# Performance work log

Measured on AMD Instinct MI355X. Metric: run time of the kernel, lower is better.

Reference implementation:

```python
import jax, jax.numpy as jnp
import numpy as np

EPS = 1e-6

def rmsnorm(x, w):
    return x * jax.lax.rsqrt(jnp.mean(x * x, axis=-1, keepdims=True) + EPS) * w

def apply_rope(q, k, freqs_cis):
    # q: (B,T,H,D), k: (B,T,Hkv,D), freqs_cis: (T, D//2, 2) = (cos, sin)
    cos = freqs_cis[None, :, None, :, 0]
    sin = freqs_cis[None, :, None, :, 1]
    def rot(t):
        tr = t.reshape(*t.shape[:-1], t.shape[-1] // 2, 2)
        re, im = tr[..., 0], tr[..., 1]
        out = jnp.stack([re * cos - im * sin, re * sin + im * cos], axis=-1)
        return out.reshape(t.shape)
    return rot(q), rot(k)

def swiglu(x, w1, w2, w3):
    # torch Linear: y = x @ W.T ; SwiGLU: (silu(x W1^T) * (x W3^T)) W2^T
    return (jax.nn.silu(x @ w1.T) * (x @ w3.T)) @ w2.T

def setup_inputs() -> dict:
    key = jax.random.key(0)
    ks = jax.random.split(key, 16)
    B, T, C = 4, 2048, 1024
    H, Hkv, D = 16, 4, 64
    E, Hh = 8, 512
    s = 0.02
    # rotary frequencies (theta=10000)
    inv_freq = 1.0 / (10000.0 ** (np.arange(0, D, 2, dtype=np.float32) / D))
    t = np.arange(T, dtype=np.float32)
    ang = np.outer(t, inv_freq)  # (T, D/2)
    freqs_cis = jnp.asarray(np.stack([np.cos(ang), np.sin(ang)], axis=-1))
    return {
        "x": jax.random.normal(ks[0], (B, T, C), jnp.float32),
        "freqs_cis": freqs_cis,
        "norm1_w": jnp.ones((C,), jnp.float32),
        "wq": jax.random.normal(ks[1], (C, C), jnp.float32) * s,
        "wk": jax.random.normal(ks[2], (Hkv * D, C), jnp.float32) * s,
        "wv": jax.random.normal(ks[3], (Hkv * D, C), jnp.float32) * s,
        "wo": jax.random.normal(ks[4], (C, C), jnp.float32) * s,
        "norm2_w": jnp.ones((C,), jnp.float32),
        "gate_w": jax.random.normal(ks[5], (E, C), jnp.float32) * s,
        "sw1": jax.random.normal(ks[6], (Hh, C), jnp.float32) * s,
        "sw2": jax.random.normal(ks[7], (C, Hh), jnp.float32) * s,
        "sw3": jax.random.normal(ks[8], (Hh, C), jnp.float32) * s,
        "ew1": jax.random.normal(ks[9], (E, Hh, C), jnp.float32) * s,
        "ew2": jax.random.normal(ks[10], (E, C, Hh), jnp.float32) * s,
        "ew3": jax.random.normal(ks[11], (E, Hh, C), jnp.float32) * s,
    }

def reference(x, freqs_cis, norm1_w, wq, wk, wv, wo, norm2_w, gate_w,
              sw1, sw2, sw3, ew1, ew2, ew3):
    B, T, C = x.shape
    H, Hkv = 16, 4
    D = C // H
    n_rep = H // Hkv
    E, top_k = gate_w.shape[0], 2

    # --- attention (GQA + RoPE, causal) ---
    xn = rmsnorm(x, norm1_w)
    q = (xn @ wq.T).reshape(B, T, H, D)
    k = (xn @ wk.T).reshape(B, T, Hkv, D)
    v = (xn @ wv.T).reshape(B, T, Hkv, D)
    q, k = apply_rope(q, k, freqs_cis)
    k = jnp.repeat(k, n_rep, axis=2)
    v = jnp.repeat(v, n_rep, axis=2)
    q, k, v = (t.transpose(0, 2, 1, 3) for t in (q, k, v))  # (B,H,T,D)
    scores = jnp.einsum("bhqd,bhkd->bhqk", q, k) / jnp.sqrt(jnp.float32(D))
    causal = jnp.tril(jnp.ones((T, T), bool))
    scores = jnp.where(causal, scores, jnp.finfo(scores.dtype).min)
    attn = jax.nn.softmax(scores, axis=-1)
    y = jnp.einsum("bhqk,bhkd->bhqd", attn, v)
    y = y.transpose(0, 2, 1, 3).reshape(B, T, C) @ wo.T
    x = x + y

    # --- MoE FFN ---
    xn2 = rmsnorm(x, norm2_w)
    shared = swiglu(xn2, sw1, sw2, sw3)
    router_logits = xn2 @ gate_w.T  # (B,T,E)
    top_logits, top_idx = jax.lax.top_k(router_logits, top_k)
    top_w = jax.nn.softmax(top_logits, axis=-1)  # (B,T,top_k)
    # dense per-expert weight, zero where not selected (same math as masked loop)
    w_full = jnp.sum(jax.nn.one_hot(top_idx, E, dtype=xn2.dtype) * top_w[..., None], axis=-2)  # (B,T,E)
    h = jax.nn.silu(jnp.einsum("btc,ehc->bteh", xn2, ew1)) * jnp.einsum("btc,ehc->bteh", xn2, ew3)
    expert_out = jnp.einsum("bteh,ech,bte->btc", h, ew2, w_full)
    x = x + shared + expert_out
    return x, router_logits
```

## Files before the change

### kernel.cpp

```cpp
#include <hip/hip_runtime.h>
#include <math.h>

typedef __bf16 bf16;
typedef bf16 bf16x8 __attribute__((ext_vector_type(8)));
typedef bf16 bf16x4 __attribute__((ext_vector_type(4)));
typedef float f32x4 __attribute__((ext_vector_type(4)));

#define B_    4
#define T_    2048
#define C_    1024
#define H_    16
#define HKV_  4
#define D_    64
#define HH_   512
#define E_    8
#define MTOK  (B_*T_)
#define MAXTILES 144
#define ROWCAP  (MAXTILES*128)

__device__ __forceinline__ f32x4 mfma16(bf16x8 a, bf16x8 b, f32x4 c) {
  return __builtin_amdgcn_mfma_f32_16x16x32_bf16(a, b, c, 0, 0, 0);
}

#define GLOAD16(gsrc, ldst) \
  __builtin_amdgcn_global_load_lds((const __attribute__((address_space(1))) void*)(gsrc), \
                                   (__attribute__((address_space(3))) void*)(ldst), 16, 0, 0)

#define XCD_SWZ(bx, by) \
  const int _nw  = gridDim.x * gridDim.y; \
  const int _bid = blockIdx.y * gridDim.x + blockIdx.x; \
  const int _swz = (_bid & 7) * (_nw >> 3) + (_bid >> 3); \
  const int bx = _swz % gridDim.x; \
  const int by = _swz / gridDim.x;

struct CastSegs {
  const float* src[10];
  bf16* dst[10];
  int prefix[11];
};
__global__ void cast_all_kernel(CastSegs cs) {
  int i = blockIdx.x * 256 + threadIdx.x;
  if (i >= cs.prefix[10]) return;
  int seg = 0;
  #pragma unroll
  for (int k = 0; k < 9; ++k) if (i >= cs.prefix[k+1]) seg = k+1;
  int j = i - cs.prefix[seg];
  float4 v = reinterpret_cast<const float4*>(cs.src[seg])[j];
  bf16x4 o = { (bf16)v.x, (bf16)v.y, (bf16)v.z, (bf16)v.w };
  reinterpret_cast<bf16x4*>(cs.dst[seg])[j] = o;
}

__global__ void rmsnorm_cast_kernel(const float* __restrict__ x, const float* __restrict__ w,
                                    bf16* __restrict__ out) {
  int row = blockIdx.x;
  const float4* xr = reinterpret_cast<const float4*>(x + (size_t)row * C_);
  float4 v = xr[threadIdx.x];
  float ss = v.x*v.x + v.y*v.y + v.z*v.z + v.w*v.w;
  #pragma unroll
  for (int off = 32; off > 0; off >>= 1) ss += __shfl_down(ss, off);
  __shared__ float red[4];
  if ((threadIdx.x & 63) == 0) red[threadIdx.x >> 6] = ss;
  __syncthreads();
  float tot = red[0] + red[1] + red[2] + red[3];
  float scale = rsqrtf(tot * (1.0f / C_) + 1e-6f);
  float4 wv = reinterpret_cast<const float4*>(w)[threadIdx.x];
  bf16x4 o = { (bf16)(v.x*scale*wv.x), (bf16)(v.y*scale*wv.y),
               (bf16)(v.z*scale*wv.z), (bf16)(v.w*scale*wv.w) };
  reinterpret_cast<bf16x4*>(out + (size_t)row * C_)[threadIdx.x] = o;
}

template<int EPI>
__global__ __launch_bounds__(256, 4)
void gemm_bt(const bf16* __restrict__ A, const bf16* __restrict__ W,
             float* __restrict__ D, const float* __restrict__ SRC,
             const float* __restrict__ RS, int rs_stride,
             int M, int N, int K)
{
  XCD_SWZ(bx, by);
  __shared__ __align__(16) bf16 As[128*64];
  __shared__ __align__(16) bf16 Bs[128*64];
  const int tid  = threadIdx.x;
  const int lane = tid & 63;
  const int wid  = tid >> 6;
  const int wr = wid >> 1, wc = wid & 1;
  const int m0 = by * 128;
  const int n0 = bx * 128;
  const int r  = lane & 15;
  const int kg = lane >> 4;
  const int sr8 = lane >> 3;
  const int sc  = ((lane & 7) ^ sr8) * 8;
  const bf16* gA = A + (size_t)(m0 + wid*32 + sr8) * K + sc;
  const bf16* gB = W + (size_t)(n0 + wid*32 + sr8) * K + sc;
  bf16* lA = As + wid * 2048;
  bf16* lB = Bs + wid * 2048;

  f32x4 acc[4][4];
  #pragma unroll
  for (int i = 0; i < 4; ++i)
    #pragma unroll
    for (int j = 0; j < 4; ++j) acc[i][j] = f32x4{0.f,0.f,0.f,0.f};

  for (int kk = 0; kk < K; kk += 64) {
    #pragma unroll
    for (int p = 0; p < 4; ++p) {
      GLOAD16(gA + (size_t)(8*p) * K + kk, lA + p*512);
      GLOAD16(gB + (size_t)(8*p) * K + kk, lB + p*512);
    }
    __syncthreads();
    #pragma unroll
    for (int ks = 0; ks < 2; ++ks) {
      const int sz = (((ks << 2) | kg) ^ (r & 7)) * 8;
      bf16x8 a[4], b[4];
      #pragma unroll
      for (int i = 0; i < 4; ++i)
        a[i] = *reinterpret_cast<const bf16x8*>(&As[(wr*64 + i*16 + r)*64 + sz]);
      #pragma unroll
      for (int j = 0; j < 4; ++j)
        b[j] = *reinterpret_cast<const bf16x8*>(&Bs[(wc*64 + j*16 + r)*64 + sz]);
      #pragma unroll
      for (int i = 0; i < 4; ++i)
        #pragma unroll
        for (int j = 0; j < 4; ++j)
          acc[i][j] = mfma16(a[i], b[j], acc[i][j]);
    }
    __syncthreads();
  }
  const int dr = kg * 4;
  #pragma unroll
  for (int i = 0; i < 4; ++i)
    #pragma unroll
    for (int j = 0; j < 4; ++j)
      #pragma unroll
      for (int rr = 0; rr < 4; ++rr) {
        int m = m0 + wr*64 + i*16 + dr + rr;
        int n = n0 + wc*64 + j*16 + r;
        size_t idx = (size_t)m * N + n;
        float v = acc[i][j][rr];
        if (EPI == 0)      D[idx] = v;
        else if (EPI == 1) D[idx] = SRC[idx] + v;
        else if (EPI == 2) D[idx] += v;
        else               D[idx] += RS[(size_t)m * rs_stride] * v;
      }
}

__global__ __launch_bounds__(256, 4)
void gemm_qkv(const bf16* __restrict__ A, const bf16* __restrict__ W,
              const float* __restrict__ fr,
              bf16* __restrict__ qb, bf16* __restrict__ kb, bf16* __restrict__ vb)
{
  const int K = C_;
  XCD_SWZ(bx, by);
  __shared__ __align__(16) bf16 As[128*64];
  __shared__ __align__(16) bf16 Bs[128*64];
  const int tid  = threadIdx.x;
  const int lane = tid & 63;
  const int wid  = tid >> 6;
  const int wr = wid >> 1, wc = wid & 1;
  const int m0 = by * 128;
  const int n0 = bx * 128;
  const int r  = lane & 15;
  const int kg = lane >> 4;
  const int sr8 = lane >> 3;
  const int sc  = ((lane & 7) ^ sr8) * 8;
  const bf16* gA = A + (size_t)(m0 + wid*32 + sr8) * K + sc;
  const bf16* gB = W + (size_t)(n0 + wid*32 + sr8) * K + sc;
  bf16* lA = As + wid * 2048;
  bf16* lB = Bs + wid * 2048;

  f32x4 acc[4][4];
  #pragma unroll
  for (int i = 0; i < 4; ++i)
    #pragma unroll
    for (int j = 0; j < 4; ++j) acc[i][j] = f32x4{0.f,0.f,0.f,0.f};

  for (int kk = 0; kk < K; kk += 64) {
    #pragma unroll
    for (int p = 0; p < 4; ++p) {
      GLOAD16(gA + (size_t)(8*p) * K + kk, lA + p*512);
      GLOAD16(gB + (size_t)(8*p) * K + kk, lB + p*512);
    }
    __syncthreads();
    #pragma unroll
    for (int ks = 0; ks < 2; ++ks) {
      const int sz = (((ks << 2) | kg) ^ (r & 7)) * 8;
      bf16x8 a[4], b[4];
      #pragma unroll
      for (int i = 0; i < 4; ++i)
        a[i] = *reinterpret_cast<const bf16x8*>(&As[(wr*64 + i*16 + r)*64 + sz]);
      #pragma unroll
      for (int j = 0; j < 4; ++j)
        b[j] = *reinterpret_cast<const bf16x8*>(&Bs[(wc*64 + j*16 + r)*64 + sz]);
      #pragma unroll
      for (int i = 0; i < 4; ++i)
        #pragma unroll
        for (int j = 0; j < 4; ++j)
          acc[i][j] = mfma16(a[i], b[j], acc[i][j]);
    }
    __syncthreads();
  }
  const float QSCALE = 0.125f * 1.44269504088896340736f;
  const int dr = kg * 4;
  #pragma unroll
  for (int i = 0; i < 4; ++i)
    #pragma unroll
    for (int j = 0; j < 4; ++j)
      #pragma unroll
      for (int rr = 0; rr < 4; ++rr) {
        int mrow = m0 + wr*64 + i*16 + dr + rr;
        int b  = mrow >> 11, t = mrow & (T_ - 1);
        int n  = n0 + wc*64 + j*16 + r;
        float v = acc[i][j][rr];
        float p = __shfl_xor(v, 1);
        if (n < 1024) {
          float c = fr[t*64 + (n & 62)], s = fr[t*64 + (n & 62) + 1];
          float ov = (n & 1) ? (p*s + v*c) : (v*c - p*s);
          qb[((size_t)(b*H_ + (n >> 6)) * T_ + t) * 64 + (n & 63)] = (bf16)(ov * QSCALE);
        } else if (n < 1280) {
          float c = fr[t*64 + (n & 62)], s = fr[t*64 + (n & 62) + 1];
          float ov = (n & 1) ? (p*s + v*c) : (v*c - p*s);
          kb[((size_t)(b*HKV_ + ((n - 1024) >> 6)) * T_ + t) * 64 + (n & 63)] = (bf16)ov;
        } else {
          vb[((size_t)(b*HKV_ + ((n - 1280) >> 6)) * T_ + t) * 64 + (n & 63)] = (bf16)v;
        }
      }
}

__global__ __launch_bounds__(256, 4)
void gemm_up_all(const bf16* __restrict__ A,
                 const bf16* __restrict__ SW1, const bf16* __restrict__ SW3,
                 const bf16* __restrict__ EW1, const bf16* __restrict__ EW3,
                 size_t wstride, bf16* __restrict__ sb, bf16* __restrict__ sbm,
                 const int* __restrict__ tb, const int* __restrict__ tki)
{
  const int K = C_;
  XCD_SWZ(bx, by);
  const int y = by;
  const bool dense = (y < 64);
  const bf16 *W1, *W3;
  int rowbase;
  bf16* outp;
  if (dense) {
    W1 = SW1; W3 = SW3; rowbase = y * 128; outp = sb;
  } else {
    int ye = y - 64;
    if (ye >= tb[16]) return;
    int g = 0;
    while (ye >= tb[g + 1]) ++g;
    W1 = EW1 + (size_t)(g & 7) * wstride;
    W3 = EW3 + (size_t)(g & 7) * wstride;
    rowbase = ye * 128; outp = sbm;
  }

  __shared__ __align__(16) bf16 As[128*64];
  __shared__ __align__(16) bf16 W1s[64*64];
  __shared__ __align__(16) bf16 W3s[64*64];
  const int tid  = threadIdx.x;
  const int lane = tid & 63;
  const int wid  = tid >> 6;
  const int wr = wid >> 1, wc = wid & 1;
  const int n0 = bx * 64;
  const int r  = lane & 15;
  const int kg = lane >> 4;
  const int sr8 = lane >> 3;
  const int sc  = ((lane & 7) ^ sr8) * 8;

  int ar[4];
  #pragma unroll
  for (int p = 0; p < 4; ++p) {
    int rw = rowbase + wid*32 + p*8 + sr8;
    ar[p] = dense ? rw : tki[rw];
  }
  const bf16* gW1 = W1 + (size_t)(n0 + wid*16 + sr8) * K + sc;
  const bf16* gW3 = W3 + (size_t)(n0 + wid*16 + sr8) * K + sc;
  bf16* lA  = As  + wid * 2048;
  bf16* lW1 = W1s + wid * 1024;
  bf16* lW3 = W3s + wid * 1024;

  f32x4 acc1[4][2], acc3[4][2];
  #pragma unroll
  for (int i = 0; i < 4; ++i)
    #pragma unroll
    for (int j = 0; j < 2; ++j) { acc1[i][j] = f32x4{0.f,0.f,0.f,0.f}; acc3[i][j] = f32x4{0.f,0.f,0.f,0.f}; }

  for (int kk = 0; kk < K; kk += 64) {
    #pragma unroll
    for (int p = 0; p < 4; ++p)
      GLOAD16(A + (size_t)ar[p] * K + sc + kk, lA + p*512);
    #pragma unroll
    for (int p = 0; p < 2; ++p) {
      GLOAD16(gW1 + (size_t)(8*p) * K + kk, lW1 + p*512);
      GLOAD16(gW3 + (size_t)(8*p) * K + kk, lW3 + p*512);
    }
    __syncthreads();
    #pragma unroll
    for (int ks = 0; ks < 2; ++ks) {
      const int sz = (((ks << 2) | kg) ^ (r & 7)) * 8;
      bf16x8 a[4], w1f[2], w3f[2];
      #pragma unroll
      for (int i = 0; i < 4; ++i)
        a[i] = *reinterpret_cast<const bf16x8*>(&As[(wr*64 + i*16 + r)*64 + sz]);
      #pragma unroll
      for (int j = 0; j < 2; ++j) {
        w1f[j] = *reinterpret_cast<const bf16x8*>(&W1s[(wc*32 + j*16 + r)*64 + sz]);
        w3f[j] = *reinterpret_cast<const bf16x8*>(&W3s[(wc*32 + j*16 + r)*64 + sz]);
      }
      #pragma unroll
      for (int i = 0; i < 4; ++i)
        #pragma unroll
        for (int j = 0; j < 2; ++j) {
          acc1[i][j] = mfma16(a[i], w1f[j], acc1[i][j]);
          acc3[i][j] = mfma16(a[i], w3f[j], acc3[i][j]);
        }
    }
    __syncthreads();
  }
  const int dr = kg * 4;
  #pragma unroll
  for (int i = 0; i < 4; ++i)
    #pragma unroll
    for (int j = 0; j < 2; ++j)
      #pragma unroll
      for (int rr = 0; rr < 4; ++rr) {
        int row = rowbase + wr*64 + i*16 + dr + rr;
        int n = n0 + wc*32 + j*16 + r;
        float v1 = acc1[i][j][rr];
        float v3 = acc3[i][j][rr];
        outp[(size_t)row * HH_ + n] = (bf16)(v1 / (1.f + __expf(-v1)) * v3);
      }
}

__global__ __launch_bounds__(256, 4)
void gemm_down_all(const bf16* __restrict__ Asb, const bf16* __restrict__ Asbm,
                   const bf16* __restrict__ SW2, const bf16* __restrict__ EW2,
                   size_t wstride, bf16* __restrict__ dd, bf16* __restrict__ dwn,
                   const int* __restrict__ tb)
{
  const int K = HH_;
  XCD_SWZ(bx, by);
  const int y = by;
  const bool dense = (y < 64);
  const bf16 *A, *W;
  int rowbase;
  if (dense) {
    A = Asb; W = SW2; rowbase = y * 128;
  } else {
    int ye = y - 64;
    if (ye >= tb[16]) return;
    int g = 0;
    while (ye >= tb[g + 1]) ++g;
    A = Asbm; W = EW2 + (size_t)(g & 7) * wstride;
    rowbase = ye * 128;
  }

  __shared__ __align__(16) bf16 As[128*64];
  __shared__ __align__(16) bf16 Bs[128*64];
  const int tid  = threadIdx.x;
  const int lane = tid & 63;
  const int wid  = tid >> 6;
  const int wr = wid >> 1, wc = wid & 1;
  const int n0 = bx * 128;
  const int r  = lane & 15;
  const int kg = lane >> 4;
  const int sr8 = lane >> 3;
  const int sc  = ((lane & 7) ^ sr8) * 8;
  const bf16* gA = A + (size_t)(rowbase + wid*32 + sr8) * K + sc;
  const bf16* gB = W + (size_t)(n0 + wid*32 + sr8) * K + sc;
  bf16* lA = As + wid * 2048;
  bf16* lB = Bs + wid * 2048;

  f32x4 acc[4][4];
  #pragma unroll
  for (int i = 0; i < 4; ++i)
    #pragma unroll
    for (int j = 0; j < 4; ++j) acc[i][j] = f32x4{0.f,0.f,0.f,0.f};

  for (int kk = 0; kk < K; kk += 64) {
    #pragma unroll
    for (int p = 0; p < 4; ++p) {
      GLOAD16(gA + (size_t)(8*p) * K + kk, lA + p*512);
      GLOAD16(gB + (size_t)(8*p) * K + kk, lB + p*512);
    }
    __syncthreads();
    #pragma unroll
    for (int ks = 0; ks < 2; ++ks) {
      const int sz = (((ks << 2) | kg) ^ (r & 7)) * 8;
      bf16x8 a[4], b[4];
      #pragma unroll
      for (int i = 0; i < 4; ++i)
        a[i] = *reinterpret_cast<const bf16x8*>(&As[(wr*64 + i*16 + r)*64 + sz]);
      #pragma unroll
      for (int j = 0; j < 4; ++j)
        b[j] = *reinterpret_cast<const bf16x8*>(&Bs[(wc*64 + j*16 + r)*64 + sz]);
      #pragma unroll
      for (int i = 0; i < 4; ++i)
        #pragma unroll
        for (int j = 0; j < 4; ++j)
          acc[i][j] = mfma16(a[i], b[j], acc[i][j]);
    }
    __syncthreads();
  }
  const int dr = kg * 4;
  bf16* outp = dense ? dd : dwn;
  #pragma unroll
  for (int i = 0; i < 4; ++i)
    #pragma unroll
    for (int j = 0; j < 4; ++j)
      #pragma unroll
      for (int rr = 0; rr < 4; ++rr) {
        int row = rowbase + wr*64 + i*16 + dr + rr;
        int n = n0 + wc*64 + j*16 + r;
        outp[(size_t)row * C_ + n] = (bf16)acc[i][j][rr];
      }
}

__global__ void moe_scatter_kernel(const bf16* __restrict__ dd,
                                   const bf16* __restrict__ dwn,
                                   const int* __restrict__ t2s,
                                   const float* __restrict__ t2w,
                                   float* __restrict__ out)
{
  int t = blockIdx.x;
  int c = threadIdx.x;
  int s0 = t2s[2*t], s1 = t2s[2*t+1];
  float w0 = t2w[2*t], w1 = t2w[2*t+1];
  bf16x4 dv = reinterpret_cast<const bf16x4*>(dd  + (size_t)t  * C_)[c];
  bf16x4 a  = reinterpret_cast<const bf16x4*>(dwn + (size_t)s0 * C_)[c];
  bf16x4 b  = reinterpret_cast<const bf16x4*>(dwn + (size_t)s1 * C_)[c];
  float4* o = reinterpret_cast<float4*>(out + (size_t)t * C_);
  float4 v = o[c];
  v.x += (float)dv[0] + w0 * (float)a[0] + w1 * (float)b[0];
  v.y += (float)dv[1] + w0 * (float)a[1] + w1 * (float)b[1];
  v.z += (float)dv[2] + w0 * (float)a[2] + w1 * (float)b[2];
  v.w += (float)dv[3] + w0 * (float)a[3] + w1 * (float)b[3];
  o[c] = v;
}

__global__ void transpose_vb_kernel(const bf16* __restrict__ vb, bf16* __restrict__ vt) {
  int idx = blockIdx.x * 256 + threadIdx.x;
  const int total = B_ * HKV_ * 64 * T_;
  if (idx >= total) return;
  int t   = idx & (T_ - 1);
  int d   = (idx >> 11) & 63;
  int kvh = (idx >> 17) & 3;
  int b   = idx >> 19;
  vt[idx] = vb[((size_t)(b*HKV_ + kvh) * T_ + t) * 64 + d];
}

__global__ __launch_bounds__(256, 4)
void flash_attn_kernel(const bf16* __restrict__ Q, const bf16* __restrict__ K,
                       const bf16* __restrict__ VT, bf16* __restrict__ Y)
{
  __shared__ __align__(16) bf16 Klds[64*64];
  __shared__ __align__(16) bf16 Vlds[64*64];
  __shared__ bf16 Plds[4][2][16][72];
  const int tid  = threadIdx.x;
  const int lane = tid & 63;
  const int wid  = tid >> 6;
  const int bid  = blockIdx.x;
  const int gw   = (bid & 7) * 64 + (bid >> 3);
  const int i    = gw & 31;
  const int kvh  = (gw >> 5) & 3;
  const int b    = gw >> 7;
  const int h    = kvh * 4 + wid;
  const int r = lane & 15;
  const int g = lane >> 4;

  const bf16* kptr = K  + ((size_t)(b*HKV_ + kvh) * T_) * 64;
  const bf16* vptr = VT + ((size_t)(b*HKV_ + kvh) * 64) * T_;

  const int srow  = tid >> 3;
  const int schnk = (tid & 7) ^ (srow & 7);
  bf16* kd0 = Klds + wid * 512;
  bf16* kd1 = Klds + 2048 + wid * 512;
  bf16* vd0 = Vlds + wid * 512;
  bf16* vd1 = Vlds + 2048 + wid * 512;

  const int swz0 = ((g    ) ^ (r & 7)) * 8;
  const int swz4 = ((g + 4) ^ (r & 7)) * 8;

  bf16x8 ones;
  #pragma unroll
  for (int z = 0; z < 8; ++z) ones[z] = (bf16)1.0f;

  #pragma unroll
  for (int pi = 0; pi < 2; ++pi) {
    const int qt = pi == 0 ? (63 - i) : i;
    const int qbase = qt * 32;
    const bf16* qptr = Q + ((size_t)(b*H_ + h) * T_ + qbase) * 64;

    bf16x8 aq[2][2];
    #pragma unroll
    for (int u = 0; u < 2; ++u) {
      aq[u][0] = *reinterpret_cast<const bf16x8*>(qptr + (size_t)(u*16 + r) * 64 + g*8);
      aq[u][1] = *reinterpret_cast<const bf16x8*>(qptr + (size_t)(u*16 + r) * 64 + 32 + g*8);
    }

    f32x4 o[2][4], ol[2];
    #pragma unroll
    for (int u = 0; u < 2; ++u) {
      ol[u] = f32x4{0.f,0.f,0.f,0.f};
      #pragma unroll
      for (int q = 0; q < 4; ++q) o[u][q] = f32x4{0.f,0.f,0.f,0.f};
    }

    for (int k0 = 0; k0 < qbase + 32; k0 += 64) {
      GLOAD16(kptr + (size_t)(k0 + srow)      * 64 + schnk*8, kd0);
      GLOAD16(kptr + (size_t)(k0 + 32 + srow) * 64 + schnk*8, kd1);
      GLOAD16(vptr + (size_t)srow        * T_ + k0 + schnk*8, vd0);
      GLOAD16(vptr + (size_t)(32 + srow) * T_ + k0 + schnk*8, vd1);
      __syncthreads();
      f32x4 s[2][4];
      __builtin_amdgcn_s_setprio(1);
      #pragma unroll
      for (int c = 0; c < 4; ++c) {
        const bf16* kb = &Klds[(c*16 + r) * 64];
        bf16x8 kf0 = *reinterpret_cast<const bf16x8*>(kb + swz0);
        bf16x8 kf1 = *reinterpret_cast<const bf16x8*>(kb + swz4);
        #pragma unroll
        for (int u = 0; u < 2; ++u) {
          s[u][c] = f32x4{0.f,0.f,0.f,0.f};
          s[u][c] = mfma16(aq[u][0], kf0, s[u][c]);
          s[u][c] = mfma16(aq[u][1], kf1, s[u][c]);
        }
      }
      __builtin_amdgcn_s_setprio(0);
      #pragma unroll
      for (int u = 0; u < 2; ++u) {
        if (k0 + 63 > qbase + u*16) {
          #pragma unroll
          for (int c = 0; c < 4; ++c)
            #pragma unroll
            for (int rr = 0; rr < 4; ++rr) {
              int q = qbase + u*16 + g*4 + rr;
              int j = k0 + c*16 + r;
              if (j > q) s[u][c][rr] = -__builtin_inff();
            }
        }
      }
      #pragma unroll
      for (int u = 0; u < 2; ++u)
        #pragma unroll
        for (int c = 0; c < 4; ++c)
          #pragma unroll
          for (int rr = 0; rr < 4; ++rr)
            Plds[wid][u][g*4+rr][c*16+r] = (bf16)__builtin_amdgcn_exp2f(s[u][c][rr]);
      bf16x8 pa[2][2];
      #pragma unroll
      for (int u = 0; u < 2; ++u) {
        pa[u][0] = *reinterpret_cast<const bf16x8*>(&Plds[wid][u][r][g*8]);
        pa[u][1] = *reinterpret_cast<const bf16x8*>(&Plds[wid][u][r][32 + g*8]);
      }
      __builtin_amdgcn_s_setprio(1);
      #pragma unroll
      for (int dt = 0; dt < 4; ++dt) {
        const bf16* vb = &Vlds[(dt*16 + r) * 64];
        bf16x8 vf0 = *reinterpret_cast<const bf16x8*>(vb + swz0);
        bf16x8 vf1 = *reinterpret_cast<const bf16x8*>(vb + swz4);
        #pragma unroll
        for (int u = 0; u < 2; ++u) {
          o[u][dt] = mfma16(pa[u][0], vf0, o[u][dt]);
          o[u][dt] = mfma16(pa[u][1], vf1, o[u][dt]);
        }
      }
      #pragma unroll
      for (int u = 0; u < 2; ++u) {
        ol[u] = mfma16(pa[u][0], ones, ol[u]);
        ol[u] = mfma16(pa[u][1], ones, ol[u]);
      }
      __builtin_amdgcn_s_setprio(0);
      __syncthreads();
    }
    #pragma unroll
    for (int u = 0; u < 2; ++u)
      #pragma unroll
      for (int rr = 0; rr < 4; ++rr) {
        float inv = 1.0f / ol[u][rr];
        int t = qbase + u*16 + g*4 + rr;
        bf16* yrow = Y + ((size_t)(b*T_ + t)) * C_ + h*64;
        #pragma unroll
        for (int dt = 0; dt < 4; ++dt)
          yrow[dt*16 + r] = (bf16)(o[u][dt][rr] * inv);
      }
  }
}

__global__ void rms2_router_kernel(const float* __restrict__ x2, const float* __restrict__ nw,
                                   const float* __restrict__ gwf,
                                   bf16* __restrict__ xn_out,
                                   float* __restrict__ logits_out,
                                   int* __restrict__ t2i, float* __restrict__ t2w)
{
  int t = blockIdx.x * 4 + (threadIdx.x >> 6);
  int lane = threadIdx.x & 63;
  const float4* xr = reinterpret_cast<const float4*>(x2 + (size_t)t * C_) + lane * 4;
  float4 v[4];
  float ss = 0.f;
  #pragma unroll
  for (int i = 0; i < 4; ++i) {
    v[i] = xr[i];
    ss += v[i].x*v[i].x + v[i].y*v[i].y + v[i].z*v[i].z + v[i].w*v[i].w;
  }
  #pragma unroll
  for (int off = 32; off > 0; off >>= 1) ss += __shfl_xor(ss, off);
  float scale = rsqrtf(ss * (1.0f / C_) + 1e-6f);
  const float4* nr = reinterpret_cast<const float4*>(nw) + lane * 4;
  float xn[16];
  #pragma unroll
  for (int i = 0; i < 4; ++i) {
    float4 wv = nr[i];
    xn[4*i+0] = v[i].x * scale * wv.x;
    xn[4*i+1] = v[i].y * scale * wv.y;
    xn[4*i+2] = v[i].z * scale * wv.z;
    xn[4*i+3] = v[i].w * scale * wv.w;
  }
  {
    bf16x8 o0, o1;
    #pragma unroll
    for (int i = 0; i < 8; ++i) { o0[i] = (bf16)xn[i]; o1[i] = (bf16)xn[8+i]; }
    bf16x8* dst = reinterpret_cast<bf16x8*>(xn_out + (size_t)t * C_ + lane * 16);
    dst[0] = o0;
    dst[1] = o1;
  }
  float lg[8];
  #pragma unroll
  for (int e = 0; e < 8; ++e) {
    const float4* gr = reinterpret_cast<const float4*>(gwf + (size_t)e * C_) + lane * 4;
    float d = 0.f;
    #pragma unroll
    for (int i = 0; i < 4; ++i) {
      float4 gv = gr[i];
      d += xn[4*i+0]*gv.x + xn[4*i+1]*gv.y + xn[4*i+2]*gv.z + xn[4*i+3]*gv.w;
    }
    #pragma unroll
    for (int off = 1; off < 64; off <<= 1) d += __shfl_xor(d, off);
    lg[e] = d;
  }
  if (lane == 0) {
    #pragma unroll
    for (int e = 0; e < 8; ++e) logits_out[(size_t)t*8 + e] = lg[e];
    int i0 = 0; float b0 = lg[0];
    #pragma unroll
    for (int e = 1; e < 8; ++e) if (lg[e] > b0) { b0 = lg[e]; i0 = e; }
    int i1 = -1; float b1 = -__builtin_inff();
    #pragma unroll
    for (int e = 0; e < 8; ++e) if (e != i0 && lg[e] > b1) { b1 = lg[e]; i1 = e; }
    float w0s = 1.f / (1.f + __expf(b1 - b0));
    float w1s = 1.f - w0s;
    t2i[2*t] = i0;  t2i[2*t+1] = i1;
    t2w[2*t] = w0s; t2w[2*t+1] = w1s;
  }
}

__global__ void moe_build_kernel(const int* __restrict__ t2i, const float* __restrict__ t2w,
                                 int* __restrict__ cnt, int* __restrict__ tb,
                                 int* __restrict__ tki, float* __restrict__ tkw,
                                 int* __restrict__ t2s)
{
  __shared__ int lcnt[16], lbase[17], lcur[16];
  const int tid = threadIdx.x;
  if (tid < 16) { lcnt[tid] = 0; lcur[tid] = 0; }
  __syncthreads();
  for (int t = tid; t < MTOK; t += 1024) {
    atomicAdd(&lcnt[t2i[2*t]],     1);
    atomicAdd(&lcnt[8 + t2i[2*t+1]], 1);
  }
  __syncthreads();
  if (tid == 0) {
    int acc = 0;
    for (int g = 0; g < 16; ++g) { lbase[g] = acc; acc += (lcnt[g] + 127) >> 7; }
    lbase[16] = acc;
    for (int g = 0; g <= 16; ++g) tb[g] = lbase[g];
  }
  if (tid < 16) cnt[tid] = lcnt[tid];
  __syncthreads();
  for (int t = tid; t < MTOK; t += 1024) {
    #pragma unroll
    for (int j = 0; j < 2; ++j) {
      int g = 8*j + t2i[2*t + j];
      int p = atomicAdd(&lcur[g], 1);
      int slot = lbase[g] * 128 + p;
      tki[slot] = t;
      tkw[slot] = t2w[2*t + j];
      t2s[2*t + j] = slot;
    }
  }
  __syncthreads();
  {
    int g = tid >> 6, lane = tid & 63;
    int cs = lcnt[g];
    int ce = (cs + 127) & ~127;
    for (int p = cs + lane; p < ce; p += 64) {
      int slot = lbase[g] * 128 + p;
      tki[slot] = 0;
      tkw[slot] = 0.f;
    }
  }
}

__global__ void silu_mul_kernel(const float* __restrict__ a, const float* __restrict__ bsrc,
                                bf16* __restrict__ out, int n4)
{
  int i = blockIdx.x * 256 + threadIdx.x;
  if (i >= n4) return;
  float4 av = reinterpret_cast<const float4*>(a)[i];
  float4 bv = reinterpret_cast<const float4*>(bsrc)[i];
  bf16x4 o = { (bf16)(av.x / (1.f + __expf(-av.x)) * bv.x),
               (bf16)(av.y / (1.f + __expf(-av.y)) * bv.y),
               (bf16)(av.z / (1.f + __expf(-av.z)) * bv.z),
               (bf16)(av.w / (1.f + __expf(-av.w)) * bv.w) };
  reinterpret_cast<bf16x4*>(out)[i] = o;
}

__global__ void build_wfull_kernel(const int* __restrict__ t2i, const float* __restrict__ t2w,
                                   float* __restrict__ wfull) {
  int t = blockIdx.x * 256 + threadIdx.x;
  if (t >= MTOK) return;
  #pragma unroll
  for (int e = 0; e < 8; ++e) wfull[(size_t)t*8 + e] = 0.f;
  wfull[(size_t)t*8 + t2i[2*t]]   = t2w[2*t];
  wfull[(size_t)t*8 + t2i[2*t+1]] = t2w[2*t+1];
}

extern "C" void kernel_launch(void* const* d_in, const int* in_sizes, int n_in,
                              void* d_out, int out_size, void* d_ws, size_t ws_size,
                              hipStream_t stream)
{
  const float* x    = (const float*)d_in[0];
  const float* fr   = (const float*)d_in[1];
  const float* n1w  = (const float*)d_in[2];
  const float* wq   = (const float*)d_in[3];
  const float* wk   = (const float*)d_in[4];
  const float* wv   = (const float*)d_in[5];
  const float* wo   = (const float*)d_in[6];
  const float* n2w  = (const float*)d_in[7];
  const float* gw   = (const float*)d_in[8];
  const float* sw1  = (const float*)d_in[9];
  const float* sw2  = (const float*)d_in[10];
  const float* sw3  = (const float*)d_in[11];
  const float* ew1  = (const float*)d_in[12];
  const float* ew2  = (const float*)d_in[13];
  const float* ew3  = (const float*)d_in[14];

  float* out    = (float*)d_out;
  float* logits = out + (size_t)MTOK * C_;

  char* ws = (char*)d_ws;
  size_t off = 0;
  auto alloc = [&](size_t bytes) { size_t o = off; off += (bytes + 255) & ~(size_t)255; return o; };

  bf16* wq_b  = (bf16*)(ws + alloc((size_t)C_*C_*2));
  bf16* wk_b  = (bf16*)(ws + alloc((size_t)HKV_*D_*C_*2));
  bf16* wv_b  = (bf16*)(ws + alloc((size_t)HKV_*D_*C_*2));
  bf16* wo_b  = (bf16*)(ws + alloc((size_t)C_*C_*2));
  bf16* sw1_b = (bf16*)(ws + alloc((size_t)HH_*C_*2));
  bf16* sw3_b = (bf16*)(ws + alloc((size_t)HH_*C_*2));
  bf16* sw2_b = (bf16*)(ws + alloc((size_t)C_*HH_*2));
  bf16* ew1_b = (bf16*)(ws + alloc((size_t)E_*HH_*C_*2));
  bf16* ew2_b = (bf16*)(ws + alloc((size_t)E_*C_*HH_*2));
  bf16* ew3_b = (bf16*)(ws + alloc((size_t)E_*HH_*C_*2));
  bf16* xn_b  = (bf16*)(ws + alloc((size_t)MTOK*C_*2));
  float* wfull= (float*)(ws + alloc((size_t)MTOK*E_*4));
  int*   t2i  = (int*)  (ws + alloc((size_t)MTOK*2*4));
  float* t2w  = (float*)(ws + alloc((size_t)MTOK*2*4));
  int*   t2s  = (int*)  (ws + alloc((size_t)MTOK*2*4));
  int*   tki  = (int*)  (ws + alloc((size_t)ROWCAP*4));
  float* tkw  = (float*)(ws + alloc((size_t)ROWCAP*4));
  int*   cnt  = (int*)  (ws + alloc(32*4));
  int*   tb   = (int*)  (ws + alloc(32*4));

  const size_t POOLSZ = 81788928;
  size_t poolbase = alloc(POOLSZ);
  char* pool = ws + poolbase;
  bf16* qb = (bf16*)(pool);
  bf16* kb = (bf16*)(pool + 33554432);
  bf16* vb = (bf16*)(pool + 41943040);
  bf16* vT = (bf16*)(pool + 50331648);
  bf16* yb = (bf16*)(pool + 58720256);
  bf16* sb  = (bf16*)(pool);
  bf16* sbm = (bf16*)(pool + 8388608);
  bf16* dwn = (bf16*)(pool + 8388608 + 18874368);
  bf16* dd  = (bf16*)(pool + 65011712);
  float* g1 = (float*)pool;
  float* g3 = g1 + (size_t)MTOK*HH_;
  bf16*  sbf = (bf16*)(pool + 58720256);

  bool sparse_ok = (ws_size >= off);

  {
    CastSegs cs;
    const float* srcs[10] = { wq, wk, wv, wo, sw1, sw3, sw2, ew1, ew2, ew3 };
    bf16* dsts[10] = { wq_b, wk_b, wv_b, wo_b, sw1_b, sw3_b, sw2_b, ew1_b, ew2_b, ew3_b };
    int n4s[10] = { C_*C_/4, HKV_*D_*C_/4, HKV_*D_*C_/4, C_*C_/4,
                    HH_*C_/4, HH_*C_/4, C_*HH_/4,
                    E_*HH_*C_/4, E_*C_*HH_/4, E_*HH_*C_/4 };
    int acc = 0;
    for (int k = 0; k < 10; ++k) { cs.src[k] = srcs[k]; cs.dst[k] = dsts[k]; cs.prefix[k] = acc; acc += n4s[k]; }
    cs.prefix[10] = acc;
    cast_all_kernel<<<(acc + 255)/256, 256, 0, stream>>>(cs);
  }

  rmsnorm_cast_kernel<<<MTOK, 256, 0, stream>>>(x, n1w, xn_b);

  gemm_qkv<<<dim3(1536/128, MTOK/128), 256, 0, stream>>>(xn_b, wq_b, fr, qb, kb, vb);
  transpose_vb_kernel<<<(B_*HKV_*64*T_)/256, 256, 0, stream>>>(vb, vT);

  flash_attn_kernel<<<B_*HKV_*(T_/64), 256, 0, stream>>>(qb, kb, vT, yb);

  gemm_bt<1><<<dim3(C_/128, MTOK/128), 256, 0, stream>>>(yb, wo_b, out, x, nullptr, 0, MTOK, C_, C_);

  rms2_router_kernel<<<MTOK/4, 256, 0, stream>>>(out, n2w, gw, xn_b, logits, t2i, t2w);

  if (sparse_ok) {
    moe_build_kernel<<<1, 1024, 0, stream>>>(t2i, t2w, cnt, tb, tki, tkw, t2s);
    gemm_up_all<<<dim3(HH_/64, 64 + MAXTILES), 256, 0, stream>>>(xn_b,
        sw1_b, sw3_b, ew1_b, ew3_b, (size_t)HH_*C_, sb, sbm, tb, tki);
    gemm_down_all<<<dim3(C_/128, 64 + MAXTILES), 256, 0, stream>>>(sb, sbm,
        sw2_b, ew2_b, (size_t)C_*HH_, dd, dwn, tb);
    moe_scatter_kernel<<<MTOK, 256, 0, stream>>>(dd, dwn, t2s, t2w, out);
  } else {
    gemm_up_all<<<dim3(HH_/64, 64), 256, 0, stream>>>(xn_b,
        sw1_b, sw3_b, ew1_b, ew3_b, (size_t)HH_*C_, sb, sbm, tb, tki);
    gemm_bt<2><<<dim3(C_/128, MTOK/128), 256, 0, stream>>>(sb, sw2_b, out, nullptr, nullptr, 0, MTOK, C_, HH_);
    build_wfull_kernel<<<MTOK/256, 256, 0, stream>>>(t2i, t2w, wfull);
    for (int e = 0; e < E_; ++e) {
      const bf16* e1 = ew1_b + (size_t)e * HH_ * C_;
      const bf16* e3 = ew3_b + (size_t)e * HH_ * C_;
      const bf16* e2 = ew2_b + (size_t)e * C_ * HH_;
      gemm_bt<0><<<dim3(HH_/128, MTOK/128), 256, 0, stream>>>(xn_b, e1, g1, nullptr, nullptr, 0, MTOK, HH_, C_);
      gemm_bt<0><<<dim3(HH_/128, MTOK/128), 256, 0, stream>>>(xn_b, e3, g3, nullptr, nullptr, 0, MTOK, HH_, C_);
      silu_mul_kernel<<<((MTOK*HH_/4) + 255)/256, 256, 0, stream>>>(g1, g3, sbf, MTOK*HH_/4);
      gemm_bt<3><<<dim3(C_/128, MTOK/128), 256, 0, stream>>>(sbf, e2, out, nullptr, wfull + e, E_, MTOK, C_, HH_);
    }
  }
}
```

Measured before the change: 316.4 us.

## Double-buffer K/V LDS tiles in flash attention to prefetch next strip

Flash attention now holds two LDS buffers for K and V. While the current 64-key strip is being computed, the next strip is loaded into the other buffer, so global load latency overlaps the MFMA work. This doubles K/V shared memory, and launch bounds drop from 4 to 3 blocks per CU, which lowers occupancy. Correctness depends on the trailing __syncthreads still present at the end of each iteration, and the async GLOAD16 semantics may need a wait before the buffer is read.

Measured after the change: 310.9 us. No clear change (-1.7%).

```diff
diff --git a/kernel.cpp b/kernel.cpp
--- a/kernel.cpp
+++ b/kernel.cpp
@@ -446,12 +446,12 @@
   vt[idx] = vb[((size_t)(b*HKV_ + kvh) * T_ + t) * 64 + d];
 }
 
-__global__ __launch_bounds__(256, 4)
+__global__ __launch_bounds__(256, 3)
 void flash_attn_kernel(const bf16* __restrict__ Q, const bf16* __restrict__ K,
                        const bf16* __restrict__ VT, bf16* __restrict__ Y)
 {
-  __shared__ __align__(16) bf16 Klds[64*64];
-  __shared__ __align__(16) bf16 Vlds[64*64];
+  __shared__ __align__(16) bf16 Klds[2][64*64];
+  __shared__ __align__(16) bf16 Vlds[2][64*64];
   __shared__ bf16 Plds[4][2][16][72];
   const int tid  = threadIdx.x;
   const int lane = tid & 63;
@@ -470,10 +470,6 @@
 
   const int srow  = tid >> 3;
   const int schnk = (tid & 7) ^ (srow & 7);
-  bf16* kd0 = Klds + wid * 512;
-  bf16* kd1 = Klds + 2048 + wid * 512;
-  bf16* vd0 = Vlds + wid * 512;
-  bf16* vd1 = Vlds + 2048 + wid * 512;
 
   const int swz0 = ((g    ) ^ (r & 7)) * 8;
   const int swz4 = ((g + 4) ^ (r & 7)) * 8;
@@ -503,24 +499,40 @@
       for (int q = 0; q < 4; ++q) o[u][q] = f32x4{0.f,0.f,0.f,0.f};
     }
 
-    for (int k0 = 0; k0 < qbase + 32; k0 += 64) {
-      GLOAD16(kptr + (size_t)(k0 + srow)      * 64 + schnk*8, kd0);
-      GLOAD16(kptr + (size_t)(k0 + 32 + srow) * 64 + schnk*8, kd1);
-      GLOAD16(vptr + (size_t)srow        * T_ + k0 + schnk*8, vd0);
-      GLOAD16(vptr + (size_t)(32 + srow) * T_ + k0 + schnk*8, vd1);
-      __syncthreads();
-      f32x4 s[2][4];
+    const int nstrip = (qbase + 32 + 63) >> 6;
+
+    {
+      const int k0 = 0;
+      GLOAD16(kptr + (size_t)(k0 + srow)      * 64 + schnk*8, &Klds[0][wid*512]);
+      GLOAD16(kptr + (size_t)(k0 + 32 + srow) * 64 + schnk*8, &Klds[0][2048 + wid*512]);
+      GLOAD16(vptr + (size_t)srow        * T_ + k0 + schnk*8, &Vlds[0][wid*512]);
+      GLOAD16(vptr + (size_t)(32 + srow) * T_ + k0 + schnk*8, &Vlds[0][2048 + wid*512]);
+    }
+    __syncthreads();
+
+    for (int s = 0; s < nstrip; ++s) {
+      const int k0  = s << 6;
+      const int cur = s & 1;
+      if (s + 1 < nstrip) {
+        const int k1 = k0 + 64;
+        const int nx = cur ^ 1;
+        GLOAD16(kptr + (size_t)(k1 + srow)      * 64 + schnk*8, &Klds[nx][wid*512]);
+        GLOAD16(kptr + (size_t)(k1 + 32 + srow) * 64 + schnk*8, &Klds[nx][2048 + wid*512]);
+        GLOAD16(vptr + (size_t)srow        * T_ + k1 + schnk*8, &Vlds[nx][wid*512]);
+        GLOAD16(vptr + (size_t)(32 + srow) * T_ + k1 + schnk*8, &Vlds[nx][2048 + wid*512]);
+      }
+      f32x4 s_[2][4];
       __builtin_amdgcn_s_setprio(1);
       #pragma unroll
       for (int c = 0; c < 4; ++c) {
-        const bf16* kb = &Klds[(c*16 + r) * 64];
+        const bf16* kb = &Klds[cur][(c*16 + r) * 64];
         bf16x8 kf0 = *reinterpret_cast<const bf16x8*>(kb + swz0);
         bf16x8 kf1 = *reinterpret_cast<const bf16x8*>(kb + swz4);
         #pragma unroll
         for (int u = 0; u < 2; ++u) {
-          s[u][c] = f32x4{0.f,0.f,0.f,0.f};
-          s[u][c] = mfma16(aq[u][0], kf0, s[u][c]);
-          s[u][c] = mfma16(aq[u][1], kf1, s[u][c]);
+          s_[u][c] = f32x4{0.f,0.f,0.f,0.f};
+          s_[u][c] = mfma16(aq[u][0], kf0, s_[u][c]);
+          s_[u][c] = mfma16(aq[u][1], kf1, s_[u][c]);
         }
       }
       __builtin_amdgcn_s_setprio(0);
@@ -533,7 +545,7 @@
             for (int rr = 0; rr < 4; ++rr) {
               int q = qbase + u*16 + g*4 + rr;
               int j = k0 + c*16 + r;
-              if (j > q) s[u][c][rr] = -__builtin_inff();
+              if (j > q) s_[u][c][rr] = -__builtin_inff();
             }
         }
       }
@@ -543,7 +555,7 @@
         for (int c = 0; c < 4; ++c)
           #pragma unroll
           for (int rr = 0; rr < 4; ++rr)
-            Plds[wid][u][g*4+rr][c*16+r] = (bf16)__builtin_amdgcn_exp2f(s[u][c][rr]);
+            Plds[wid][u][g*4+rr][c*16+r] = (bf16)__builtin_amdgcn_exp2f(s_[u][c][rr]);
       bf16x8 pa[2][2];
       #pragma unroll
       for (int u = 0; u < 2; ++u) {
@@ -553,7 +565,7 @@
       __builtin_amdgcn_s_setprio(1);
       #pragma unroll
       for (int dt = 0; dt < 4; ++dt) {
-        const bf16* vb = &Vlds[(dt*16 + r) * 64];
+        const bf16* vb = &Vlds[cur][(dt*16 + r) * 64];
         bf16x8 vf0 = *reinterpret_cast<const bf16x8*>(vb + swz0);
         bf16x8 vf1 = *reinterpret_cast<const bf16x8*>(vb + swz4);
         #pragma unroll
```
